# Performance work log

Measured on AMD Instinct MI355X. Metric: run time of the kernel, lower is better.

The kernel has to match this reference:

```python
import jax, jax.numpy as jnp
import numpy as np

B, T, D, H = 4, 2048, 1024, 16
HD = D // H  # 64
LOCAL_CTX, BLOCKSIZE, VERTSIZE = 256, 1, 16
STRIDE = LOCAL_CTX // BLOCKSIZE  # 256


def build_fixed_mask(n):
    # num_verts == 1 branch of generate_fixed_attention_mask
    layout = np.zeros((n, n), dtype=np.bool_)
    # vertical stripes: top `vertsize` indices of each stride block
    for idx in range(STRIDE - VERTSIZE, STRIDE):
        layout[:, idx::STRIDE] = True
    rows = np.arange(n)
    # local: each query attends to its own stride-block
    same_block = (rows[:, None] // STRIDE) == (rows[None, :] // STRIDE)
    layout |= same_block
    # causal: zero out k > q
    layout &= rows[None, :] <= rows[:, None]
    return layout


def setup_inputs() -> dict:
    key = jax.random.key(0)
    k1, k2, k3, k4, k5 = jax.random.split(key, 5)
    s = 0.02
    return {
        "x": jax.random.normal(k1, (B, T, D), dtype=jnp.float32),
        "Wqkv": jax.random.normal(k2, (D, 3 * D), dtype=jnp.float32) * s,
        "bqkv": jax.random.normal(k3, (3 * D,), dtype=jnp.float32) * s,
        "Wproj": jax.random.normal(k4, (D, D), dtype=jnp.float32) * s,
        "bproj": jax.random.normal(k5, (D,), dtype=jnp.float32) * s,
        "mask": jnp.asarray(build_fixed_mask(T)),
    }


def reference(x, Wqkv, bqkv, Wproj, bproj, mask):
    b, t, _ = x.shape
    qkv = (x @ Wqkv + bqkv).reshape(b, t, 3, H, HD)
    # (B,T,3,H,HD) -> (B,H,T,HD) per component
    q = qkv[:, :, 0].transpose(0, 2, 1, 3)
    k = qkv[:, :, 1].transpose(0, 2, 1, 3)
    v = qkv[:, :, 2].transpose(0, 2, 1, 3)
    att = jnp.einsum("bhqd,bhkd->bhqk", q, k) * (1.0 / jnp.sqrt(jnp.float32(HD)))
    att = jnp.where(mask[:t, :t], att, -jnp.inf)
    att = jax.nn.softmax(att, axis=-1)
    y = jnp.einsum("bhqk,bhkd->bhqd", att, v)
    y = y.transpose(0, 2, 1, 3).reshape(b, t, D)
    return y @ Wproj + bproj
```

## Files before the change

### kernel.cpp

```cpp
#include <hip/hip_runtime.h>
#include <cstdint>
#include <cstddef>

typedef unsigned short u16;
typedef __attribute__((ext_vector_type(8))) short short8;
typedef __attribute__((ext_vector_type(4))) float f32x4;
typedef __attribute__((ext_vector_type(4))) unsigned short u16x4;

#define B_ 4
#define T_ 2048
#define D_ 1024
#define H_ 16
#define HD_ 64

__device__ __forceinline__ u16 f2bf(float f) {
  union { float f; unsigned i; } v; v.f = f;
  unsigned r = (v.i + 0x7FFFu + ((v.i >> 16) & 1u)) >> 16;
  return (u16)r;
}

__device__ __forceinline__ unsigned cvt_pk_bf16(float lo, float hi) {
  unsigned r;
  asm("v_cvt_pk_bf16_f32 %0, %1, %2" : "=v"(r) : "v"(lo), "v"(hi));
  return r;
}

__device__ __forceinline__ void load_lds16(const void* g, void* l) {
  __builtin_amdgcn_global_load_lds(
      (const __attribute__((address_space(1))) void*)g,
      (__attribute__((address_space(3))) void*)l, 16, 0, 0);
}

#define RBAR() asm volatile("s_barrier" ::: "memory")
#define VMC(n) asm volatile("s_waitcnt vmcnt(" #n ")" ::: "memory")

__global__ __launch_bounds__(256)
void pre_all(const float* __restrict__ x, u16* __restrict__ xb,
             const float* __restrict__ Wqkv, u16* __restrict__ WqkvT,
             const float* __restrict__ Wproj, u16* __restrict__ WprojT) {
  __shared__ u16 t[32][33];
  const int bid = blockIdx.x;
  const int tid = threadIdx.x;
  if (bid < 8192) {
    const size_t i = ((size_t)bid * 256 + tid) * 4;
    const f32x4 v = *(const f32x4*)(x + i);
    union { unsigned u[2]; u16x4 v4; } o;
    o.u[0] = cvt_pk_bf16(v[0], v[1]);
    o.u[1] = cvt_pk_bf16(v[2], v[3]);
    *(u16x4*)(xb + i) = o.v4;
    return;
  }
  const float* src; u16* dst; int R, C, bx, by;
  if (bid < 11264) {
    const int tb = bid - 8192;
    bx = tb % 96; by = tb / 96; src = Wqkv; dst = WqkvT; R = 1024; C = 3072;
  } else {
    const int tb = bid - 11264;
    bx = tb & 31; by = tb >> 5; src = Wproj; dst = WprojT; R = 1024; C = 1024;
  }
  const int c0 = bx * 32, r0 = by * 32;
  const int lr = tid >> 5, lc = tid & 31;
#pragma unroll
  for (int p = 0; p < 4; ++p)
    t[lr + p * 8][lc] = f2bf(src[(size_t)(r0 + lr + p * 8) * C + c0 + lc]);
  __syncthreads();
#pragma unroll
  for (int p = 0; p < 4; ++p)
    dst[(size_t)(c0 + lr + p * 8) * R + r0 + lc] = t[lc][lr + p * 8];
}

template <int EPI>
__global__ __launch_bounds__(256)
void gemm_db(const u16* __restrict__ A, const u16* __restrict__ Bt,
             const float* __restrict__ bias, int K, int N,
             void* __restrict__ o0v, u16* __restrict__ o1, u16* __restrict__ o2) {
  __shared__ u16 As[3][4096];
  __shared__ u16 Bs[3][4096];
  const int tid = threadIdx.x;
  const int lane = tid & 63;
  const int w = tid >> 6;
  const int q = lane >> 4, col = lane & 15;

  const int id = blockIdx.y * gridDim.x + blockIdx.x;
  const int x = id & 7;
  const int c = id >> 3;
  const int n0 = (c >> 3) * 128;
  const int m0 = ((x << 3) + (c & 7)) * 128;

  const int wm = (w >> 1) * 64, wn = (w & 1) * 64;

  const int srow = tid >> 2;
  const int cb8 = ((tid & 3) ^ ((tid >> 3) & 3)) << 3;
  const u16* Ap = A + (size_t)(m0 + srow) * K + cb8;
  const u16* Bp = Bt + (size_t)(n0 + srow) * K + cb8;

  const int rs = (q ^ ((col >> 1) & 3)) << 3;

  f32x4 acc[4][4] = {};

  auto STAGE = [&](int b, int kb) {
    load_lds16(Ap + kb, &As[b][tid * 8]);
    load_lds16(Ap + (size_t)64 * K + kb, &As[b][2048 + tid * 8]);
    load_lds16(Bp + kb, &Bs[b][tid * 8]);
    load_lds16(Bp + (size_t)64 * K + kb, &Bs[b][2048 + tid * 8]);
  };

  const int NT = K >> 5;
  STAGE(0, 0);
  STAGE(1, 32);
  int cur = 0, stg = 2;

  for (int t = 0; t < NT; ++t) {
    if (t + 2 < NT) {
      STAGE(stg, (t + 2) << 5);
      VMC(8);
    } else if (t + 1 < NT) {
      VMC(4);
    } else {
      VMC(0);
    }
    RBAR();
    short8 af[4], bfr[4];
#pragma unroll
    for (int i = 0; i < 4; ++i)
      af[i] = *(const short8*)&As[cur][(wm + i * 16 + col) * 32 + rs];
#pragma unroll
    for (int j = 0; j < 4; ++j)
      bfr[j] = *(const short8*)&Bs[cur][(wn + j * 16 + col) * 32 + rs];
#pragma unroll
    for (int i = 0; i < 4; ++i)
#pragma unroll
      for (int j = 0; j < 4; ++j)
        acc[i][j] = __builtin_amdgcn_mfma_f32_16x16x32_bf16(af[i], bfr[j], acc[i][j], 0, 0, 0);
    RBAR();
    cur = (cur == 2) ? 0 : cur + 1;
    stg = (stg == 2) ? 0 : stg + 1;
  }

#pragma unroll
  for (int j = 0; j < 4; ++j) {
    const int n = n0 + wn + j * 16 + col;
    const float bv = bias[n];
    if constexpr (EPI == 0) {
      u16* q0p = (u16*)o0v;
      const int cc = n >> 10, rem = n & 1023, hh = rem >> 6, dd = rem & 63;
#pragma unroll
      for (int i = 0; i < 4; ++i) {
        const int mrow = m0 + wm + i * 16 + q * 4;
        const int b = mrow >> 11, t = mrow & 2047;
        const int bh = b * H_ + hh;
        if (cc == 0) {
#pragma unroll
          for (int r = 0; r < 4; ++r)
            q0p[((size_t)bh * T_ + t + r) * HD_ + dd] = f2bf((acc[i][j][r] + bv) * 0.125f);
        } else if (cc == 1) {
#pragma unroll
          for (int r = 0; r < 4; ++r)
            o1[((size_t)bh * T_ + t + r) * HD_ + dd] = f2bf(acc[i][j][r] + bv);
        } else {
          union { unsigned u[2]; u16x4 v4; } pk;
          pk.u[0] = cvt_pk_bf16(acc[i][j][0] + bv, acc[i][j][1] + bv);
          pk.u[1] = cvt_pk_bf16(acc[i][j][2] + bv, acc[i][j][3] + bv);
          *(u16x4*)&o2[((size_t)bh * HD_ + dd) * T_ + t] = pk.v4;
        }
      }
    } else {
      float* outp = (float*)o0v;
#pragma unroll
      for (int i = 0; i < 4; ++i) {
        const int mrow = m0 + wm + i * 16 + q * 4;
#pragma unroll
        for (int r = 0; r < 4; ++r)
          outp[(size_t)(mrow + r) * N + n] = acc[i][j][r] + bv;
      }
    }
  }
}

__global__ __launch_bounds__(256)
void sparse_attn(const u16* __restrict__ Qb, const u16* __restrict__ Kb,
                 const u16* __restrict__ Vt, u16* __restrict__ Y) {
  __shared__ char smem[20480];
  u16* Pall = (u16*)smem;
  float* Obuf = (float*)smem;

  const int tid = threadIdx.x, lane = tid & 63, w = tid >> 6;
  const int q = lane >> 4, col = lane & 15;
  const int bh = blockIdx.x, qt = blockIdx.y;
  const int b = bh >> 4, hh = bh & 15;
  const int qb = qt >> 2;
  const int rb = (qt & 3) * 64;
  const int qg = qt * 64;
  const u16* Qh = Qb + (size_t)bh * T_ * HD_;
  const u16* Kh = Kb + (size_t)bh * T_ * HD_;
  const u16* Vh = Vt + (size_t)bh * HD_ * T_;

  short8 qf[4][2];
#pragma unroll
  for (int i = 0; i < 4; ++i)
#pragma unroll
    for (int h2 = 0; h2 < 2; ++h2)
      qf[i][h2] = *(const short8*)&Qh[(size_t)(qg + i * 16 + col) * HD_ + h2 * 32 + q * 8];

  f32x4 o[4][4] = {};
  f32x4 lI[4] = {};
  const short8 ones = {0x3F80, 0x3F80, 0x3F80, 0x3F80, 0x3F80, 0x3F80, 0x3F80, 0x3F80};

  u16* P = Pall + w * 2560;

  const int ns = (qb + 1) >> 1;
  const int L = ns + 2 * (qt & 3) + 2;

  auto params = [&](int j, int& k0, int& k1, bool& mask1, int& localc) {
    if (j < ns) {
      k0 = (2 * j) * 256 + 240; k1 = k0 + 256;
      mask1 = (2 * j + 1 == qb); localc = -1;
    } else {
      const int c = j - ns;
      k0 = qb * 256 + c * 32; k1 = k0 + 16;
      mask1 = false; localc = c * 32;
    }
  };
  auto ldK = [&](int k0, int k1, short8* kf) {
    kf[0] = *(const short8*)&Kh[(size_t)(k0 + col) * HD_ + q * 8];
    kf[1] = *(const short8*)&Kh[(size_t)(k0 + col) * HD_ + 32 + q * 8];
    kf[2] = *(const short8*)&Kh[(size_t)(k1 + col) * HD_ + q * 8];
    kf[3] = *(const short8*)&Kh[(size_t)(k1 + col) * HD_ + 32 + q * 8];
  };

  int k0 = 0, k1 = 0, localc = -1;
  bool mask1 = false;
  short8 kf[4];
  if (w < L) { params(w, k0, k1, mask1, localc); ldK(k0, k1, kf); }

  for (int j = w; j < L; j += 4) {
    const int kvb = (q < 2) ? (k0 + q * 8) : (k1 + (q - 2) * 8);
    short8 vf[4];
#pragma unroll
    for (int dt = 0; dt < 4; ++dt)
      vf[dt] = *(const short8*)&Vh[(size_t)(dt * 16 + col) * T_ + kvb];
    int nk0 = 0, nk1 = 0, nlocalc = -1;
    bool nmask1 = false;
    short8 nkf[4];
    const bool hn = (j + 4) < L;
    if (hn) { params(j + 4, nk0, nk1, nmask1, nlocalc); ldK(nk0, nk1, nkf); }

#pragma unroll
    for (int rt = 0; rt < 4; ++rt) {
      f32x4 z = {0.f, 0.f, 0.f, 0.f};
      f32x4 s0 = __builtin_amdgcn_mfma_f32_16x16x32_bf16(qf[rt][0], kf[0], z, 0, 0, 0);
      s0 = __builtin_amdgcn_mfma_f32_16x16x32_bf16(qf[rt][1], kf[1], s0, 0, 0, 0);
      f32x4 s1 = __builtin_amdgcn_mfma_f32_16x16x32_bf16(qf[rt][0], kf[2], z, 0, 0, 0);
      s1 = __builtin_amdgcn_mfma_f32_16x16x32_bf16(qf[rt][1], kf[3], s1, 0, 0, 0);
#pragma unroll
      for (int r = 0; r < 4; ++r) {
        float p0 = __expf(s0[r]);
        float p1 = mask1 ? 0.f : __expf(s1[r]);
        if (localc >= 0) {
          const int qr = rb + rt * 16 + q * 4 + r;
          if (localc + col > qr) p0 = 0.f;
          if (localc + 16 + col > qr) p1 = 0.f;
        }
        const unsigned pc = cvt_pk_bf16(p0, p1);
        P[(rt * 16 + q * 4 + r) * 40 + col] = (u16)pc;
        P[(rt * 16 + q * 4 + r) * 40 + 16 + col] = (u16)(pc >> 16);
      }
    }
    asm volatile("s_waitcnt lgkmcnt(0)" ::: "memory");
    short8 pf[4];
#pragma unroll
    for (int rt = 0; rt < 4; ++rt)
      pf[rt] = *(const short8*)&P[(rt * 16 + col) * 40 + q * 8];
#pragma unroll
    for (int rt = 0; rt < 4; ++rt) {
#pragma unroll
      for (int dt = 0; dt < 4; ++dt)
        o[rt][dt] = __builtin_amdgcn_mfma_f32_16x16x32_bf16(pf[rt], vf[dt], o[rt][dt], 0, 0, 0);
      lI[rt] = __builtin_amdgcn_mfma_f32_16x16x32_bf16(pf[rt], ones, lI[rt], 0, 0, 0);
    }
    if (hn) {
      k0 = nk0; k1 = nk1; mask1 = nmask1; localc = nlocalc;
      kf[0] = nkf[0]; kf[1] = nkf[1]; kf[2] = nkf[2]; kf[3] = nkf[3];
    }
  }

#pragma unroll
  for (int rt = 0; rt < 4; ++rt) {
    __syncthreads();
#pragma unroll
    for (int dt = 0; dt < 4; ++dt)
      *(f32x4*)&Obuf[(w * 65 + dt * 16 + col) * 16 + q * 4] = o[rt][dt];
    if (col == 0)
      *(f32x4*)&Obuf[(w * 65 + 64) * 16 + q * 4] = lI[rt];
    __syncthreads();
    f32x4 acc = {0.f, 0.f, 0.f, 0.f};
    f32x4 lt = {0.f, 0.f, 0.f, 0.f};
#pragma unroll
    for (int w2 = 0; w2 < 4; ++w2) {
      acc += *(const f32x4*)&Obuf[(w2 * 65 + w * 16 + col) * 16 + q * 4];
      lt += *(const f32x4*)&Obuf[(w2 * 65 + 64) * 16 + q * 4];
    }
#pragma unroll
    for (int r = 0; r < 4; ++r) {
      const int trow = qg + rt * 16 + q * 4 + r;
      Y[((size_t)(b * T_ + trow)) * D_ + hh * HD_ + w * 16 + col] = f2bf(acc[r] / lt[r]);
    }
  }
}

extern "C" void kernel_launch(void* const* d_in, const int* in_sizes, int n_in,
                              void* d_out, int out_size, void* d_ws, size_t ws_size,
                              hipStream_t stream) {
  const float* x = (const float*)d_in[0];
  const float* Wqkv = (const float*)d_in[1];
  const float* bqkv = (const float*)d_in[2];
  const float* Wproj = (const float*)d_in[3];
  const float* bproj = (const float*)d_in[4];
  float* out = (float*)d_out;

  char* ws = (char*)d_ws;
  u16* xb     = (u16*)(ws + 0);
  u16* WqkvT  = (u16*)(ws + 16777216);
  u16* WprojT = (u16*)(ws + 23068672);
  u16* Qb     = (u16*)(ws + 25165824);
  u16* Kb     = (u16*)(ws + 41943040);
  u16* Vt     = (u16*)(ws + 58720256);
  u16* Y      = (u16*)(ws + 75497472);

  pre_all<<<dim3(12288), 256, 0, stream>>>(x, xb, Wqkv, WqkvT, Wproj, WprojT);
  gemm_db<0><<<dim3(24, 64), 256, 0, stream>>>(xb, WqkvT, bqkv, 1024, 3072, Qb, Kb, Vt);
  sparse_attn<<<dim3(64, 32), 256, 0, stream>>>(Qb, Kb, Vt, Y);
  gemm_db<1><<<dim3(8, 64), 256, 0, stream>>>(Y, WprojT, bproj, 1024, 1024, out, nullptr, nullptr);
}
```

Before: 243.1 us.

## Add dedicated triple-buffered 256x128 GEMM kernel for output projection

Replaces the generic double-buffered GEMM used for the output projection with a specialized kernel. The new kernel uses 512 threads, 256x128 tiles, a three-stage LDS pipeline with swizzled reads, and a grouped block-index mapping for L2 locality. The aim is more data reuse per tile and better latency hiding for the 8192x1024x1024 projection. It fixes the grid at 256 blocks, so it is specialized to these shapes, and it uses more LDS per block, which limits occupancy.

Result: no change. 247.2 us (+1.7%).

```diff
diff --git a/kernel.cpp b/kernel.cpp
--- a/kernel.cpp
+++ b/kernel.cpp
@@ -177,6 +177,86 @@
   }
 }
 
+__global__ __launch_bounds__(512, 2)
+void gemm_proj(const u16* __restrict__ A, const u16* __restrict__ Bt,
+               const float* __restrict__ bias, int K, int N,
+               float* __restrict__ out) {
+  __shared__ u16 As[3][8192];
+  __shared__ u16 Bs[3][4096];
+  const int tid = threadIdx.x;
+  const int lane = tid & 63;
+  const int w = tid >> 6;
+  const int q = lane >> 4, col = lane & 15;
+
+  const int id = blockIdx.x;
+  const int x = id & 7;
+  const int c = id >> 3;
+  const int m0 = ((x << 2) + (c >> 3)) * 256;
+  const int n0 = (c & 7) * 128;
+
+  const int wm = (w & 3) * 64, wn = (w >> 2) * 64;
+
+  const int srow = tid >> 2;
+  const int cb8 = ((tid & 3) ^ ((tid >> 3) & 3)) << 3;
+  const u16* Ap = A + (size_t)(m0 + srow) * K + cb8;
+  const u16* Bp = Bt + (size_t)(n0 + srow) * K + cb8;
+
+  const int rs = (q ^ ((col >> 1) & 3)) << 3;
+
+  f32x4 acc[4][4] = {};
+
+  auto STAGE = [&](int b, int kb) {
+    load_lds16(Ap + kb, &As[b][tid * 8]);
+    load_lds16(Ap + (size_t)128 * K + kb, &As[b][4096 + tid * 8]);
+    load_lds16(Bp + kb, &Bs[b][tid * 8]);
+  };
+
+  const int NT = K >> 5;
+  STAGE(0, 0);
+  STAGE(1, 32);
+  int cur = 0, stg = 2;
+
+  for (int t = 0; t < NT; ++t) {
+    if (t + 2 < NT) {
+      STAGE(stg, (t + 2) << 5);
+      VMC(6);
+    } else if (t + 1 < NT) {
+      VMC(3);
+    } else {
+      VMC(0);
+    }
+    RBAR();
+    short8 af[4], bfr[4];
+#pragma unroll
+    for (int i = 0; i < 4; ++i)
+      af[i] = *(const short8*)&As[cur][(wm + i * 16 + col) * 32 + rs];
+#pragma unroll
+    for (int j = 0; j < 4; ++j)
+      bfr[j] = *(const short8*)&Bs[cur][(wn + j * 16 + col) * 32 + rs];
+#pragma unroll
+    for (int i = 0; i < 4; ++i)
+#pragma unroll
+      for (int j = 0; j < 4; ++j)
+        acc[i][j] = __builtin_amdgcn_mfma_f32_16x16x32_bf16(af[i], bfr[j], acc[i][j], 0, 0, 0);
+    RBAR();
+    cur = (cur == 2) ? 0 : cur + 1;
+    stg = (stg == 2) ? 0 : stg + 1;
+  }
+
+#pragma unroll
+  for (int j = 0; j < 4; ++j) {
+    const int n = n0 + wn + j * 16 + col;
+    const float bv = bias[n];
+#pragma unroll
+    for (int i = 0; i < 4; ++i) {
+      const int mrow = m0 + wm + i * 16 + q * 4;
+#pragma unroll
+      for (int r = 0; r < 4; ++r)
+        out[(size_t)(mrow + r) * N + n] = acc[i][j][r] + bv;
+    }
+  }
+}
+
 __global__ __launch_bounds__(256)
 void sparse_attn(const u16* __restrict__ Qb, const u16* __restrict__ Kb,
                  const u16* __restrict__ Vt, u16* __restrict__ Y) {
@@ -330,5 +410,5 @@
   pre_all<<<dim3(12288), 256, 0, stream>>>(x, xb, Wqkv, WqkvT, Wproj, WprojT);
   gemm_db<0><<<dim3(24, 64), 256, 0, stream>>>(xb, WqkvT, bqkv, 1024, 3072, Qb, Kb, Vt);
   sparse_attn<<<dim3(64, 32), 256, 0, stream>>>(Qb, Kb, Vt, Y);
-  gemm_db<1><<<dim3(8, 64), 256, 0, stream>>>(Y, WprojT, bproj, 1024, 1024, out, nullptr, nullptr);
-}
+  gemm_proj<<<dim3(256), 512, 0, stream>>>(Y, WprojT, bproj, 1024, 1024, out);
+}
```
